# Performance work log

Hardware: AMD Instinct MI355X
Metric: run time of the kernel (lower is better)

Reference implementation:

```python
import jax, jax.numpy as jnp
import numpy as np

BONE_NUM = 16
THRESH = 0.7


def masked_l2(out, tar, mask):
    # out, tar: [B, C, H, W]; mask: [B, H, W]
    diff_norm = jnp.linalg.norm(out - tar, axis=1)          # [B, H, W]
    masked = jnp.where(mask > THRESH, diff_norm, 0.0)
    B = out.shape[0]
    flat_m = masked.reshape(B, -1)
    flat_d = diff_norm.reshape(B, -1)
    cnt = jnp.sum(flat_m != 0, axis=1)                       # device-side nonzero count
    per_sample = jnp.where(
        cnt > 0,
        flat_m.sum(axis=1) / jnp.maximum(cnt, 1).astype(flat_m.dtype),
        flat_d.mean(axis=1),
    )
    return per_sample.mean()


def pose_nocs_loss(pred_joint_map, pred_joint_score, out_mask, tar_joints):
    # pred_joint_map: [B, bn*3, H, W]; pred_joint_score: [B, bn, H, W]
    # out_mask: [B, H, W]; tar_joints: [B, bn, 3]
    B, _, H, W = pred_joint_map.shape
    bn = BONE_NUM
    jm = pred_joint_map.reshape(B, bn, 3, H, W) * out_mask[:, None, None]
    score = jax.nn.sigmoid(pred_joint_score) * out_mask[:, None]        # [B, bn, H, W]
    denom = score.reshape(B, bn, -1).sum(axis=2)[:, :, None, None] + 1e-5
    score_map = score / denom
    jm = jax.lax.stop_gradient(jm) * score_map[:, :, None]              # [B, bn, 3, H, W]
    pred_joint = jm.reshape(B, bn, 3, -1).sum(axis=3)                   # [B, bn, 3]
    loss = jnp.linalg.norm(pred_joint - tar_joints, axis=2).sum()
    return loss / (B * bn)


def setup_inputs() -> dict:
    key = jax.random.key(0)
    k1, k2, k3 = jax.random.split(key, 3)
    B, H, W = 4, 256, 256
    bn = BONE_NUM
    output = jax.random.normal(k1, (B, 4 + bn * 8 + 2, H, W), dtype=jnp.float32)
    tar_maps = jax.random.uniform(k2, (B, 4 + bn * 6 + 1, H, W), dtype=jnp.float32)
    tar_pose = jax.random.normal(k3, (B, bn, 6), dtype=jnp.float32)
    return {"output": output, "tar_maps": tar_maps, "tar_pose": tar_pose}


def reference(output, tar_maps, tar_pose):
    bn = BONE_NUM
    B = output.shape[0]

    # --- slice predictions ---
    pred_nocs = output[:, 0:3]
    mask_logits = output[:, 3]                                # sigmoid applied below
    pred_loc_map = jax.nn.sigmoid(output[:, 4:4 + bn * 3])
    pred_rot_map = jax.nn.sigmoid(output[:, 4 + bn * 3:4 + bn * 6])
    pred_skin_seg = output[:, 4 + bn * 6:4 + bn * 7 + 2]       # [B, bn+2, H, W]
    pred_joint_score = output[:, 4 + bn * 7 + 2:4 + bn * 8 + 2]  # [B, bn, H, W]

    # --- slice targets ---
    target_nocs = tar_maps[:, 0:3]
    target_mask = tar_maps[:, 3]
    tar_loc_map = jax.nn.sigmoid(tar_maps[:, 4:4 + bn * 3])
    tar_rot_map = jax.nn.sigmoid(tar_maps[:, 4 + bn * 3:4 + bn * 6])
    tar_skin_seg = tar_maps[:, 4 + bn * 6].astype(jnp.int32)   # [B, H, W]
    tar_loc = jax.nn.sigmoid(tar_pose[:, :, 0:3])
    tar_rot = jax.nn.sigmoid(tar_pose[:, :, 3:6])

    # --- BCE mask loss (on sigmoid(mask_logits) vs target_mask), stable form ---
    mask_loss = -jnp.mean(
        target_mask * jax.nn.log_sigmoid(mask_logits)
        + (1.0 - target_mask) * jax.nn.log_sigmoid(-mask_logits)
    )

    # --- masked L2 losses ---
    nocs_loss = masked_l2(pred_nocs, target_nocs, target_mask)
    loc_map_loss = masked_l2(pred_loc_map, tar_loc_map, target_mask)
    rot_map_loss = masked_l2(pred_rot_map, tar_rot_map, target_mask)

    # --- skinning cross entropy ---
    logits = jnp.transpose(pred_skin_seg, (0, 2, 3, 1)).reshape(-1, bn + 2)
    labels = tar_skin_seg.reshape(-1)
    logp = jax.nn.log_softmax(logits, axis=-1)
    skin_loss = -jnp.mean(jnp.take_along_axis(logp, labels[:, None], axis=1))

    # --- pose losses ---
    loc_loss = pose_nocs_loss(pred_loc_map, pred_joint_score, target_mask, tar_loc)
    rot_loss = pose_nocs_loss(pred_rot_map, pred_joint_score, target_mask, tar_rot)

    return jnp.stack([nocs_loss, mask_loss, loc_loss, loc_map_loss,
                      rot_loss, rot_map_loss, skin_loss])
```

## Files before the change

kernel.cpp:

```cpp
#include <hip/hip_runtime.h>
#include <math.h>

#define HW 65536
#define BN 16


__device__ __forceinline__ float fsig(float x) {
    return __builtin_amdgcn_rcpf(1.0f + __expf(-x));
}
__device__ __forceinline__ float sq(float x) { return x * x; }

__device__ __forceinline__ float wred(float v) {
#pragma unroll
    for (int off = 32; off; off >>= 1) v += __shfl_xor(v, off, 64);
    return v;
}

__global__ __launch_bounds__(256) void mvpm_fused(const float* __restrict__ outp,
                                                  const float* __restrict__ tarp,
                                                  float* __restrict__ ws) {
    const int b = blockIdx.y;
    const int p = blockIdx.x * 256 + threadIdx.x;
    const float* ob = outp + (size_t)b * 134 * HW + p;
    const float* tb = tarp + (size_t)b * 101 * HW + p;
    const int lane = threadIdx.x & 63;
    const int wv = threadIdx.x >> 6;

    __shared__ float jacc[BN][7][4];
    __shared__ float red[11][4];

    const float m  = tb[3 * HW];
    const float ml = ob[3 * HW];
    const float a0 = ob[0], a1 = ob[HW], a2 = ob[2 * HW];
    const float b0 = tb[0], b1 = tb[HW], b2 = tb[2 * HW];

    const float bce = m * fminf(ml, 0.0f) + (1.0f - m) * fminf(-ml, 0.0f)
                      - __logf(1.0f + __expf(-fabsf(ml)));
    const float dn = sqrtf(sq(a0 - b0) + sq(a1 - b1) + sq(a2 - b2));
    const bool sel = m > 0.7f;
    const float mm = m * m;

    float x[18];
#pragma unroll
    for (int k = 0; k < 18; ++k) x[k] = ob[(100 + k) * HW];
    const float labf = tb[100 * HW];
    float mx = x[0];
#pragma unroll
    for (int k = 1; k < 18; ++k) mx = fmaxf(mx, x[k]);
    float se = 0.0f;
#pragma unroll
    for (int k = 0; k < 18; ++k) se += __expf(x[k] - mx);
    int lab = (int)labf; lab = lab < 0 ? 0 : (lab > 17 ? 17 : lab);
    float xl = x[0];
#pragma unroll
    for (int k = 1; k < 18; ++k) xl = (lab == k) ? x[k] : xl;
    const float skin = mx + __logf(se) - xl;

    float dsl = 0.0f, dsr = 0.0f;
#pragma unroll 2
    for (int j = 0; j < BN; ++j) {
        const int cl = (4 + 3 * j) * HW, cr = (52 + 3 * j) * HW;
        const float o0 = ob[cl], o1 = ob[cl + HW], o2 = ob[cl + 2 * HW];
        const float t0 = tb[cl], t1 = tb[cl + HW], t2 = tb[cl + 2 * HW];
        const float p0 = ob[cr], p1 = ob[cr + HW], p2 = ob[cr + 2 * HW];
        const float q0 = tb[cr], q1 = tb[cr + HW], q2 = tb[cr + 2 * HW];
        const float sc = ob[(118 + j) * HW];

        const float so0 = fsig(o0), so1 = fsig(o1), so2 = fsig(o2);
        const float sp0 = fsig(p0), sp1 = fsig(p1), sp2 = fsig(p2);
        dsl += sq(so0 - fsig(t0)) + sq(so1 - fsig(t1)) + sq(so2 - fsig(t2));
        dsr += sq(sp0 - fsig(q0)) + sq(sp1 - fsig(q1)) + sq(sp2 - fsig(q2));

        const float ss = fsig(sc);
        const float w2 = ss * mm;
        float u[7];
        u[0] = ss * m;
        u[1] = so0 * w2; u[2] = so1 * w2; u[3] = so2 * w2;
        u[4] = sp0 * w2; u[5] = sp1 * w2; u[6] = sp2 * w2;

#pragma unroll
        for (int off = 32; off; off >>= 1) {
#pragma unroll
            for (int i = 0; i < 7; ++i) u[i] += __shfl_xor(u[i], off, 64);
        }
        if (lane == 0) {
#pragma unroll
            for (int i = 0; i < 7; ++i) jacc[j][i][wv] = u[i];
        }
    }
    const float dnl = sqrtf(dsl), dnr = sqrtf(dsr);

    float v[11];
    v[0]  = bce;
    v[1]  = skin;
    v[2]  = sel ? dn : 0.0f;
    v[3]  = (sel && dn != 0.0f) ? 1.0f : 0.0f;
    v[4]  = dn;
    v[5]  = sel ? dnl : 0.0f;
    v[6]  = (sel && dnl != 0.0f) ? 1.0f : 0.0f;
    v[7]  = dnl;
    v[8]  = sel ? dnr : 0.0f;
    v[9]  = (sel && dnr != 0.0f) ? 1.0f : 0.0f;
    v[10] = dnr;

#pragma unroll
    for (int off = 32; off; off >>= 1) {
#pragma unroll
        for (int i = 0; i < 11; ++i) v[i] += __shfl_xor(v[i], off, 64);
    }
    if (lane == 0) {
#pragma unroll
        for (int i = 0; i < 11; ++i) red[i][wv] = v[i];
    }
    __syncthreads();

    const int t = threadIdx.x;
    if (t < 112) {
        const int j = t / 7, c = t % 7;
        const float s = jacc[j][c][0] + jacc[j][c][1] + jacc[j][c][2] + jacc[j][c][3];
        atomicAdd(&ws[38 + (b * 16 + j) * 7 + c], s);
    } else if (t >= 128 && t < 139) {
        const int i = t - 128;
        const float s = red[i][0] + red[i][1] + red[i][2] + red[i][3];
        const int g = (i < 2) ? i : (2 + b * 9 + (i - 2));
        atomicAdd(&ws[g], s);
    }
}

__global__ __launch_bounds__(64) void mvpm_fin(const float* __restrict__ ws,
                                               const float* __restrict__ tp,
                                               float* __restrict__ o) {
    const int t = threadIdx.x;
    const int base = 38 + t * 7;

    float S = ws[base] + 1e-5f;
    float ln = 0.0f, rn = 0.0f;
#pragma unroll
    for (int c = 0; c < 3; ++c) {
        float pl = ws[base + 1 + c] / S;
        float tl = 1.0f / (1.0f + expf(-tp[t * 6 + c]));
        ln += (pl - tl) * (pl - tl);
        float pr = ws[base + 4 + c] / S;
        float tr = 1.0f / (1.0f + expf(-tp[t * 6 + 3 + c]));
        rn += (pr - tr) * (pr - tr);
    }
    ln = sqrtf(ln);
    rn = sqrtf(rn);
    float lsum = wred(ln);
    float rsum = wred(rn);

    if (t == 0) {
        float nocs = 0.0f, locm = 0.0f, rotm = 0.0f;
        for (int bb = 0; bb < 4; ++bb) {
            int ba = 2 + bb * 9;
            nocs += (ws[ba + 1] > 0.5f) ? ws[ba + 0] / ws[ba + 1] : ws[ba + 2] * (1.0f / HW);
            locm += (ws[ba + 4] > 0.5f) ? ws[ba + 3] / ws[ba + 4] : ws[ba + 5] * (1.0f / HW);
            rotm += (ws[ba + 7] > 0.5f) ? ws[ba + 6] / ws[ba + 7] : ws[ba + 8] * (1.0f / HW);
        }
        o[0] = nocs * 0.25f;
        o[1] = -ws[0] / (4.0f * HW);
        o[2] = lsum * (1.0f / 64.0f);
        o[3] = locm * 0.25f;
        o[4] = rsum * (1.0f / 64.0f);
        o[5] = rotm * 0.25f;
        o[6] = ws[1] / (4.0f * HW);
    }
}

extern "C" void kernel_launch(void* const* d_in, const int* in_sizes, int n_in,
                              void* d_out, int out_size, void* d_ws, size_t ws_size,
                              hipStream_t stream) {
    const float* outp = (const float*)d_in[0];
    const float* tarp = (const float*)d_in[1];
    const float* tpos = (const float*)d_in[2];
    float* o  = (float*)d_out;
    float* ws = (float*)d_ws;

    hipMemsetAsync(d_ws, 0, 486 * sizeof(float), stream);
    dim3 g(HW / 256, 4);
    mvpm_fused<<<g, 256, 0, stream>>>(outp, tarp, ws);
    mvpm_fin<<<1, 64, 0, stream>>>(ws, tpos, o);
}
```

Measured before the change: 284.6 us.

## Process four pixels per thread with float4 loads and pre-reduce before shuffles

Result: no change. 279.3 us (-1.9%).

```diff
diff --git a/kernel.cpp b/kernel.cpp
--- a/kernel.cpp
+++ b/kernel.cpp
@@ -3,6 +3,7 @@
 
 #define HW 65536
 #define BN 16
+#define C4 (HW / 4)
 
 
 __device__ __forceinline__ float fsig(float x) {
@@ -14,69 +15,91 @@
 #pragma unroll
     for (int off = 32; off; off >>= 1) v += __shfl_xor(v, off, 64);
     return v;
+}
+__device__ __forceinline__ float4 fsig4(float4 a) {
+    return make_float4(fsig(a.x), fsig(a.y), fsig(a.z), fsig(a.w));
 }
 
 __global__ __launch_bounds__(256) void mvpm_fused(const float* __restrict__ outp,
                                                   const float* __restrict__ tarp,
                                                   float* __restrict__ ws) {
     const int b = blockIdx.y;
-    const int p = blockIdx.x * 256 + threadIdx.x;
-    const float* ob = outp + (size_t)b * 134 * HW + p;
-    const float* tb = tarp + (size_t)b * 101 * HW + p;
+    const int idx = blockIdx.x * 256 + threadIdx.x;
+    const float4* ob = (const float4*)(outp + (size_t)b * 134 * HW) + idx;
+    const float4* tb = (const float4*)(tarp + (size_t)b * 101 * HW) + idx;
     const int lane = threadIdx.x & 63;
     const int wv = threadIdx.x >> 6;
 
     __shared__ float jacc[BN][7][4];
     __shared__ float red[11][4];
 
-    const float m  = tb[3 * HW];
-    const float ml = ob[3 * HW];
-    const float a0 = ob[0], a1 = ob[HW], a2 = ob[2 * HW];
-    const float b0 = tb[0], b1 = tb[HW], b2 = tb[2 * HW];
-
-    const float bce = m * fminf(ml, 0.0f) + (1.0f - m) * fminf(-ml, 0.0f)
-                      - __logf(1.0f + __expf(-fabsf(ml)));
-    const float dn = sqrtf(sq(a0 - b0) + sq(a1 - b1) + sq(a2 - b2));
-    const bool sel = m > 0.7f;
-    const float mm = m * m;
-
-    float x[18];
-#pragma unroll
-    for (int k = 0; k < 18; ++k) x[k] = ob[(100 + k) * HW];
-    const float labf = tb[100 * HW];
-    float mx = x[0];
-#pragma unroll
-    for (int k = 1; k < 18; ++k) mx = fmaxf(mx, x[k]);
-    float se = 0.0f;
-#pragma unroll
-    for (int k = 0; k < 18; ++k) se += __expf(x[k] - mx);
-    int lab = (int)labf; lab = lab < 0 ? 0 : (lab > 17 ? 17 : lab);
-    float xl = x[0];
-#pragma unroll
-    for (int k = 1; k < 18; ++k) xl = (lab == k) ? x[k] : xl;
-    const float skin = mx + __logf(se) - xl;
-
-    float dsl = 0.0f, dsr = 0.0f;
+    const float4 fm = tb[3 * C4];
+    const float4 ml = ob[3 * C4];
+    const float4 a0 = ob[0], a1 = ob[C4], a2 = ob[2 * C4];
+    const float4 b0 = tb[0], b1 = tb[C4], b2 = tb[2 * C4];
+
+    float bce = 0.0f;
+#define BCE1(c) bce += fm.c * fminf(ml.c, 0.0f) + (1.0f - fm.c) * fminf(-ml.c, 0.0f) \
+                       - __logf(1.0f + __expf(-fabsf(ml.c)));
+    BCE1(x) BCE1(y) BCE1(z) BCE1(w)
+#undef BCE1
+
+    float4 dn;
+    dn.x = sqrtf(sq(a0.x - b0.x) + sq(a1.x - b1.x) + sq(a2.x - b2.x));
+    dn.y = sqrtf(sq(a0.y - b0.y) + sq(a1.y - b1.y) + sq(a2.y - b2.y));
+    dn.z = sqrtf(sq(a0.z - b0.z) + sq(a1.z - b1.z) + sq(a2.z - b2.z));
+    dn.w = sqrtf(sq(a0.w - b0.w) + sq(a1.w - b1.w) + sq(a2.w - b2.w));
+    const float4 mm = make_float4(fm.x * fm.x, fm.y * fm.y, fm.z * fm.z, fm.w * fm.w);
+
+    float4 xx[18];
+#pragma unroll
+    for (int k = 0; k < 18; ++k) xx[k] = ob[(100 + k) * C4];
+    const float4 labf = tb[100 * C4];
+    float skin = 0.0f;
+#define SKIN1(c) {                                                             \
+        float mx = xx[0].c;                                                    \
+        _Pragma("unroll")                                                      \
+        for (int k = 1; k < 18; ++k) mx = fmaxf(mx, xx[k].c);                  \
+        float se = 0.0f;                                                       \
+        _Pragma("unroll")                                                      \
+        for (int k = 0; k < 18; ++k) se += __expf(xx[k].c - mx);               \
+        int lab = (int)labf.c; lab = lab < 0 ? 0 : (lab > 17 ? 17 : lab);      \
+        float xl = xx[0].c;                                                    \
+        _Pragma("unroll")                                                      \
+        for (int k = 1; k < 18; ++k) xl = (lab == k) ? xx[k].c : xl;           \
+        skin += mx + __logf(se) - xl; }
+    SKIN1(x) SKIN1(y) SKIN1(z) SKIN1(w)
+#undef SKIN1
+
+    float4 dsl = make_float4(0.f, 0.f, 0.f, 0.f);
+    float4 dsr = make_float4(0.f, 0.f, 0.f, 0.f);
 #pragma unroll 2
     for (int j = 0; j < BN; ++j) {
-        const int cl = (4 + 3 * j) * HW, cr = (52 + 3 * j) * HW;
-        const float o0 = ob[cl], o1 = ob[cl + HW], o2 = ob[cl + 2 * HW];
-        const float t0 = tb[cl], t1 = tb[cl + HW], t2 = tb[cl + 2 * HW];
-        const float p0 = ob[cr], p1 = ob[cr + HW], p2 = ob[cr + 2 * HW];
-        const float q0 = tb[cr], q1 = tb[cr + HW], q2 = tb[cr + 2 * HW];
-        const float sc = ob[(118 + j) * HW];
-
-        const float so0 = fsig(o0), so1 = fsig(o1), so2 = fsig(o2);
-        const float sp0 = fsig(p0), sp1 = fsig(p1), sp2 = fsig(p2);
-        dsl += sq(so0 - fsig(t0)) + sq(so1 - fsig(t1)) + sq(so2 - fsig(t2));
-        dsr += sq(sp0 - fsig(q0)) + sq(sp1 - fsig(q1)) + sq(sp2 - fsig(q2));
-
-        const float ss = fsig(sc);
-        const float w2 = ss * mm;
+        const int cl = (4 + 3 * j) * C4, cr = (52 + 3 * j) * C4;
+        const float4 o0 = ob[cl], o1 = ob[cl + C4], o2 = ob[cl + 2 * C4];
+        const float4 t0 = tb[cl], t1 = tb[cl + C4], t2 = tb[cl + 2 * C4];
+        const float4 p0 = ob[cr], p1 = ob[cr + C4], p2 = ob[cr + 2 * C4];
+        const float4 q0 = tb[cr], q1 = tb[cr + C4], q2 = tb[cr + 2 * C4];
+        const float4 sc = ob[(118 + j) * C4];
+
+        const float4 so0 = fsig4(o0), so1 = fsig4(o1), so2 = fsig4(o2);
+        const float4 sp0 = fsig4(p0), sp1 = fsig4(p1), sp2 = fsig4(p2);
+        const float4 st0 = fsig4(t0), st1 = fsig4(t1), st2 = fsig4(t2);
+        const float4 uq0 = fsig4(q0), uq1 = fsig4(q1), uq2 = fsig4(q2);
+        const float4 ss = fsig4(sc);
+
+#define ACCJ(c) dsl.c += sq(so0.c - st0.c) + sq(so1.c - st1.c) + sq(so2.c - st2.c); \
+                dsr.c += sq(sp0.c - uq0.c) + sq(sp1.c - uq1.c) + sq(sp2.c - uq2.c);
+        ACCJ(x) ACCJ(y) ACCJ(z) ACCJ(w)
+#undef ACCJ
+
+        const float4 w4 = make_float4(ss.x * mm.x, ss.y * mm.y, ss.z * mm.z, ss.w * mm.w);
         float u[7];
-        u[0] = ss * m;
-        u[1] = so0 * w2; u[2] = so1 * w2; u[3] = so2 * w2;
-        u[4] = sp0 * w2; u[5] = sp1 * w2; u[6] = sp2 * w2;
+        u[0] = ss.x * fm.x + ss.y * fm.y + ss.z * fm.z + ss.w * fm.w;
+#define DOT4(v4) (v4.x * w4.x + v4.y * w4.y + v4.z * w4.z + v4.w * w4.w)
+        u[1] = DOT4(so0); u[2] = DOT4(so1); u[3] = DOT4(so2);
+        u[4] = DOT4(sp0); u[5] = DOT4(sp1); u[6] = DOT4(sp2);
+#undef DOT4
 
 #pragma unroll
         for (int off = 32; off; off >>= 1) {
@@ -88,20 +111,29 @@
             for (int i = 0; i < 7; ++i) jacc[j][i][wv] = u[i];
         }
     }
-    const float dnl = sqrtf(dsl), dnr = sqrtf(dsr);
+
+    float4 dnl, dnr;
+    dnl.x = sqrtf(dsl.x); dnl.y = sqrtf(dsl.y); dnl.z = sqrtf(dsl.z); dnl.w = sqrtf(dsl.w);
+    dnr.x = sqrtf(dsr.x); dnr.y = sqrtf(dsr.y); dnr.z = sqrtf(dsr.z); dnr.w = sqrtf(dsr.w);
 
     float v[11];
-    v[0]  = bce;
-    v[1]  = skin;
-    v[2]  = sel ? dn : 0.0f;
-    v[3]  = (sel && dn != 0.0f) ? 1.0f : 0.0f;
-    v[4]  = dn;
-    v[5]  = sel ? dnl : 0.0f;
-    v[6]  = (sel && dnl != 0.0f) ? 1.0f : 0.0f;
-    v[7]  = dnl;
-    v[8]  = sel ? dnr : 0.0f;
-    v[9]  = (sel && dnr != 0.0f) ? 1.0f : 0.0f;
-    v[10] = dnr;
+    v[0] = bce;
+    v[1] = skin;
+#pragma unroll
+    for (int i = 2; i < 11; ++i) v[i] = 0.0f;
+#define PIX1(c) {                                                              \
+        const bool sel = fm.c > 0.7f;                                          \
+        v[2]  += sel ? dn.c : 0.0f;                                            \
+        v[3]  += (sel && dn.c != 0.0f) ? 1.0f : 0.0f;                          \
+        v[4]  += dn.c;                                                         \
+        v[5]  += sel ? dnl.c : 0.0f;                                           \
+        v[6]  += (sel && dnl.c != 0.0f) ? 1.0f : 0.0f;                         \
+        v[7]  += dnl.c;                                                        \
+        v[8]  += sel ? dnr.c : 0.0f;                                           \
+        v[9]  += (sel && dnr.c != 0.0f) ? 1.0f : 0.0f;                         \
+        v[10] += dnr.c; }
+    PIX1(x) PIX1(y) PIX1(z) PIX1(w)
+#undef PIX1
 
 #pragma unroll
     for (int off = 32; off; off >>= 1) {
@@ -177,7 +209,7 @@
     float* ws = (float*)d_ws;
 
     hipMemsetAsync(d_ws, 0, 486 * sizeof(float), stream);
-    dim3 g(HW / 256, 4);
+    dim3 g(HW / 1024, 4);
     mvpm_fused<<<g, 256, 0, stream>>>(outp, tarp, ws);
     mvpm_fin<<<1, 64, 0, stream>>>(ws, tpos, o);
 }
```
